# Optimization experiments

Hardware: AMD Instinct MI355X
Metric: run time of the kernel (lower is better)

The kernel has to match this reference:

```python
import jax, jax.numpy as jnp
import numpy as np

NUM_LAYERS = 25
INPUT = 500
HIDDEN = 64
SEQ = 25
BATCH = 4096
OUT = 10
GATES = 4 * HIDDEN


def setup_inputs() -> dict:
    key = jax.random.key(0)
    ks = jax.random.split(key, 11)
    s = 0.1  # ~ uniform(-1/sqrt(H),1/sqrt(H)) scale used by torch LSTM init
    return {
        "x": jax.random.normal(ks[0], (SEQ, BATCH, INPUT), jnp.float32),
        "W_ih0": jax.random.normal(ks[1], (GATES, INPUT), jnp.float32) * s,
        "W_hh0": jax.random.normal(ks[2], (GATES, HIDDEN), jnp.float32) * s,
        "b_ih0": jax.random.normal(ks[3], (GATES,), jnp.float32) * s,
        "b_hh0": jax.random.normal(ks[4], (GATES,), jnp.float32) * s,
        "W_ih_rest": jax.random.normal(ks[5], (NUM_LAYERS - 1, GATES, HIDDEN), jnp.float32) * s,
        "W_hh_rest": jax.random.normal(ks[6], (NUM_LAYERS - 1, GATES, HIDDEN), jnp.float32) * s,
        "b_ih_rest": jax.random.normal(ks[7], (NUM_LAYERS - 1, GATES), jnp.float32) * s,
        "b_hh_rest": jax.random.normal(ks[8], (NUM_LAYERS - 1, GATES), jnp.float32) * s,
        "W_lin": jax.random.normal(ks[9], (OUT, HIDDEN), jnp.float32) * s,
        "b_lin": jax.random.normal(ks[10], (OUT,), jnp.float32) * s,
    }


def _lstm_layer(seq, Wih, Whh, bih, bhh):
    # seq: [T, B, D_in] -> (outputs [T, B, H], h_T [B, H], c_T [B, H])
    T, B, _ = seq.shape
    H = Whh.shape[1]
    # precompute input projection for all timesteps in one big GEMM
    xp = jnp.einsum('tbi,gi->tbg', seq, Wih) + bih + bhh  # [T, B, 4H]
    h0 = jnp.zeros((B, H), seq.dtype)
    c0 = jnp.zeros((B, H), seq.dtype)

    def step(carry, xpt):
        h, c = carry
        g = xpt + h @ Whh.T  # [B, 4H], torch gate order i, f, g, o
        i, f, gg, o = jnp.split(g, 4, axis=-1)
        c = jax.nn.sigmoid(f) * c + jax.nn.sigmoid(i) * jnp.tanh(gg)
        h = jax.nn.sigmoid(o) * jnp.tanh(c)
        return (h, c), h

    (hT, cT), hs = jax.lax.scan(step, (h0, c0), xp)
    return hs, hT, cT


def reference(x, W_ih0, W_hh0, b_ih0, b_hh0, W_ih_rest, W_hh_rest, b_ih_rest, b_hh_rest, W_lin, b_lin):
    hs, hT, cT = _lstm_layer(x, W_ih0, W_hh0, b_ih0, b_hh0)
    h_list, c_list = [hT], [cT]
    for l in range(NUM_LAYERS - 1):  # fixed small layer count: Python loop ok
        hs, hT, cT = _lstm_layer(hs, W_ih_rest[l], W_hh_rest[l], b_ih_rest[l], b_hh_rest[l])
        h_list.append(hT)
        c_list.append(cT)
    h_n = jnp.stack(h_list)  # [L, B, H]
    c_n = jnp.stack(c_list)  # [L, B, H]
    # faithful to torch: out[:, -1, :] indexes the BATCH dim -> [T, H]
    lstm_out = hs[:, -1, :] @ W_lin.T + b_lin  # [T, OUT]
    return (lstm_out, h_n, c_n)
```

## Files before the change

### kernel.cpp

```cpp
#include <hip/hip_runtime.h>

#define T_SEQ 25
#define NBATCH 4096
#define D_IN 500
#define HID 64
#define NG 256
#define NLAYERS 25
#define NOUT 10

typedef __attribute__((ext_vector_type(8))) short bf16x8;
typedef __attribute__((ext_vector_type(4))) short bf16x4;
typedef __attribute__((ext_vector_type(4))) float f32x4;

#define LOG2E 1.4426950408889634f

__device__ __forceinline__ short f2bf(float f) {
    union { float f; unsigned u; } v; v.f = f;
    unsigned u = v.u + 0x7FFFu + ((v.u >> 16) & 1u);
    return (short)(u >> 16);
}
__device__ __forceinline__ float bf2f(short s) {
    union { unsigned u; float f; } v;
    v.u = ((unsigned)(unsigned short)s) << 16;
    return v.f;
}
__device__ __forceinline__ bf16x8 cvt8(f32x4 a, f32x4 b) {
    bf16x8 r;
    r[0]=f2bf(a[0]); r[1]=f2bf(a[1]); r[2]=f2bf(a[2]); r[3]=f2bf(a[3]);
    r[4]=f2bf(b[0]); r[5]=f2bf(b[1]); r[6]=f2bf(b[2]); r[7]=f2bf(b[3]);
    return r;
}
__device__ __forceinline__ float sigm(float x) {
    return __builtin_amdgcn_rcpf(1.f + __builtin_amdgcn_exp2f(-LOG2E * x));
}
__device__ __forceinline__ float tanh_f(float x) {
    return 1.f - 2.f * __builtin_amdgcn_rcpf(__builtin_amdgcn_exp2f(2.f * LOG2E * x) + 1.f);
}

__global__ __launch_bounds__(256)
void prep(const float* __restrict__ Wih0, const float* __restrict__ Whh0,
          const float* __restrict__ WihR, const float* __restrict__ WhhR,
          const float* __restrict__ bihR, const float* __restrict__ bhhR,
          short* __restrict__ wbf, short* __restrict__ whh0b,
          short* __restrict__ wihRb, short* __restrict__ whhRb,
          float* __restrict__ bsum) {
    int idx = blockIdx.x * 256 + threadIdx.x;
    if (idx < 131072) {
        int row = idx >> 9, k = idx & 511;
        wbf[idx] = (k < D_IN) ? f2bf(Wih0[row * D_IN + k]) : (short)0;
    } else if (idx < 147456) {
        int j = idx - 131072; whh0b[j] = f2bf(Whh0[j]);
    } else if (idx < 540672) {
        int j = idx - 147456; wihRb[j] = f2bf(WihR[j]);
    } else if (idx < 933888) {
        int j = idx - 540672; whhRb[j] = f2bf(WhhR[j]);
    } else if (idx < 940032) {
        int j = idx - 933888; bsum[j] = bihR[j] + bhhR[j];
    }
}

__global__ __launch_bounds__(256, 1)
void xp0_gemm(const float* __restrict__ x, const short* __restrict__ wbf,
              const float* __restrict__ bih0, const float* __restrict__ bhh0,
              short* __restrict__ xp0b) {
    const int tid = threadIdx.x;
    const int wv = tid >> 6, lane = tid & 63, col = lane & 15, q = lane >> 4;
    const int t  = blockIdx.x >> 5;
    const int b0 = (blockIdx.x & 31) << 7;

    f32x4 acc[2][16];
    #pragma unroll
    for (int nt = 0; nt < 16; nt++) {
        int g = nt*16 + col;
        float bv = bih0[g] + bhh0[g];
        acc[0][nt] = (f32x4){bv,bv,bv,bv};
        acc[1][nt] = acc[0][nt];
    }
    const float* xrow0 = x + ((size_t)t*NBATCH + b0 + wv*32 + col)*D_IN;
    const float* xrow1 = xrow0 + 16*(size_t)D_IN;

    #pragma unroll 3
    for (int kc = 0; kc < 15; kc++) {
        const int ko = kc*32 + q*8;
        const f32x4* p0 = (const f32x4*)(xrow0 + ko);
        const f32x4* p1 = (const f32x4*)(xrow1 + ko);
        bf16x8 a0 = cvt8(p0[0], p0[1]);
        bf16x8 a1 = cvt8(p1[0], p1[1]);
        #pragma unroll
        for (int nt = 0; nt < 16; nt++) {
            bf16x8 bfr = *(const bf16x8*)(wbf + (size_t)(nt*16+col)*512 + kc*32 + q*8);
            acc[0][nt] = __builtin_amdgcn_mfma_f32_16x16x32_bf16(a0, bfr, acc[0][nt], 0,0,0);
            acc[1][nt] = __builtin_amdgcn_mfma_f32_16x16x32_bf16(a1, bfr, acc[1][nt], 0,0,0);
        }
    }
    {
        f32x4 z = (f32x4){0.f,0.f,0.f,0.f};
        f32x4 lo0=z, hi0=z, lo1=z, hi1=z;
        const int ko = 480 + q*8;
        if (q < 2) {
            lo0 = *(const f32x4*)(xrow0 + ko); hi0 = *(const f32x4*)(xrow0 + ko + 4);
            lo1 = *(const f32x4*)(xrow1 + ko); hi1 = *(const f32x4*)(xrow1 + ko + 4);
        } else if (q == 2) {
            lo0 = *(const f32x4*)(xrow0 + 496);
            lo1 = *(const f32x4*)(xrow1 + 496);
        }
        bf16x8 a0 = cvt8(lo0, hi0);
        bf16x8 a1 = cvt8(lo1, hi1);
        #pragma unroll
        for (int nt = 0; nt < 16; nt++) {
            bf16x8 bfr = *(const bf16x8*)(wbf + (size_t)(nt*16+col)*512 + 480 + q*8);
            acc[0][nt] = __builtin_amdgcn_mfma_f32_16x16x32_bf16(a0, bfr, acc[0][nt], 0,0,0);
            acc[1][nt] = __builtin_amdgcn_mfma_f32_16x16x32_bf16(a1, bfr, acc[1][nt], 0,0,0);
        }
    }
    #pragma unroll
    for (int ms = 0; ms < 2; ms++) {
        #pragma unroll
        for (int nt = 0; nt < 16; nt++) {
            int g = nt*16 + col;
            int b = b0 + wv*32 + ms*16 + q*4;
            bf16x4 o;
            o[0]=f2bf(acc[ms][nt][0]); o[1]=f2bf(acc[ms][nt][1]);
            o[2]=f2bf(acc[ms][nt][2]); o[3]=f2bf(acc[ms][nt][3]);
            *(bf16x4*)(xp0b + ((size_t)t*NG + g)*NBATCH + b) = o;
        }
    }
}

__global__ __launch_bounds__(256, 1)
void lstm_persist(const short* __restrict__ whh0b, const short* __restrict__ wihRb,
                  const short* __restrict__ whhRb, const float* __restrict__ bsum,
                  const float* __restrict__ Wlin, const float* __restrict__ blin,
                  const short* __restrict__ xp0b, float* __restrict__ out) {
    __shared__ short seq[T_SEQ * 16 * 72];
    const int tid = threadIdx.x;
    const int wv = tid >> 6, lane = tid & 63, col = lane & 15, q = lane >> 4;
    const int b0 = blockIdx.x << 4;
    const int hh = wv*16 + col;
    float* __restrict__ h_n = out + 250;
    float* __restrict__ c_n = out + 250 + (size_t)NLAYERS*NBATCH*HID;

    bf16x8 wih[4][2], whh[4][2];
    float bias[4];

    #pragma unroll 1
    for (int l = 0; l < NLAYERS; l++) {
        if (l == 0) {
            #pragma unroll
            for (int gt = 0; gt < 4; gt++) {
                const short* wr = whh0b + (size_t)(gt*64 + hh)*64;
                whh[gt][0] = *(const bf16x8*)(wr + q*8);
                whh[gt][1] = *(const bf16x8*)(wr + 32 + q*8);
            }
        } else {
            const short* wi = wihRb + (size_t)(l-1)*16384;
            const short* wh = whhRb + (size_t)(l-1)*16384;
            #pragma unroll
            for (int gt = 0; gt < 4; gt++) {
                int g = gt*64 + hh;
                wih[gt][0] = *(const bf16x8*)(wi + (size_t)g*64 + q*8);
                wih[gt][1] = *(const bf16x8*)(wi + (size_t)g*64 + 32 + q*8);
                whh[gt][0] = *(const bf16x8*)(wh + (size_t)g*64 + q*8);
                whh[gt][1] = *(const bf16x8*)(wh + (size_t)g*64 + 32 + q*8);
                bias[gt] = bsum[(size_t)(l-1)*NG + g];
            }
        }
        float c[4] = {0.f, 0.f, 0.f, 0.f};

        #pragma unroll 1
        for (int j = 0; j < 5; j++) {
            const int t0 = j*5;
            f32x4 pre[5][4];
            if (l == 0) {
                #pragma unroll
                for (int i = 0; i < 5; i++) {
                    #pragma unroll
                    for (int gt = 0; gt < 4; gt++) {
                        bf16x4 v = *(const bf16x4*)(xp0b +
                            ((size_t)(t0+i)*NG + gt*64 + hh)*NBATCH + b0 + q*4);
                        f32x4 p;
                        p[0]=bf2f(v[0]); p[1]=bf2f(v[1]); p[2]=bf2f(v[2]); p[3]=bf2f(v[3]);
                        pre[i][gt] = p;
                    }
                }
            } else {
                #pragma unroll
                for (int i = 0; i < 5; i++) {
                    const short* sp = &seq[((t0+i)*16 + col)*72];
                    bf16x8 a0 = *(const bf16x8*)(sp + q*8);
                    bf16x8 a1 = *(const bf16x8*)(sp + 32 + q*8);
                    #pragma unroll
                    for (int gt = 0; gt < 4; gt++) {
                        f32x4 p = (f32x4){bias[gt],bias[gt],bias[gt],bias[gt]};
                        p = __builtin_amdgcn_mfma_f32_16x16x32_bf16(a0, wih[gt][0], p, 0,0,0);
                        p = __builtin_amdgcn_mfma_f32_16x16x32_bf16(a1, wih[gt][1], p, 0,0,0);
                        pre[i][gt] = p;
                    }
                }
            }
            __syncthreads();

            #pragma unroll
            for (int i = 0; i < 5; i++) {
                const int t = t0 + i;
                f32x4 acc4[4];
                #pragma unroll
                for (int gt = 0; gt < 4; gt++) acc4[gt] = pre[i][gt];
                if (i > 0 || j > 0) {
                    const short* hp = &seq[((t-1)*16 + col)*72];
                    bf16x8 h0 = *(const bf16x8*)(hp + q*8);
                    bf16x8 h1 = *(const bf16x8*)(hp + 32 + q*8);
                    #pragma unroll
                    for (int gt = 0; gt < 4; gt++) {
                        acc4[gt] = __builtin_amdgcn_mfma_f32_16x16x32_bf16(h0, whh[gt][0], acc4[gt], 0,0,0);
                        acc4[gt] = __builtin_amdgcn_mfma_f32_16x16x32_bf16(h1, whh[gt][1], acc4[gt], 0,0,0);
                    }
                }
                #pragma unroll
                for (int r = 0; r < 4; r++) {
                    float ig = sigm(acc4[0][r]);
                    float fg = sigm(acc4[1][r]);
                    float gg = tanh_f(acc4[2][r]);
                    float og = sigm(acc4[3][r]);
                    float cn = fg*c[r] + ig*gg;
                    c[r] = cn;
                    float hn = og * tanh_f(cn);
                    seq[(t*16 + q*4 + r)*72 + hh] = f2bf(hn);
                    if (i == 4) {
                        if (t == T_SEQ-1) {
                            size_t o = ((size_t)l*NBATCH + b0 + q*4 + r)*HID + hh;
                            h_n[o] = hn;
                            c_n[o] = cn;
                        }
                    }
                }
                __syncthreads();
            }
        }
    }
    if (b0 == NBATCH - 16 && tid < T_SEQ*NOUT) {
        int ti = tid / NOUT, o = tid - ti*NOUT;
        float s = blin[o];
        #pragma unroll
        for (int k = 0; k < HID; k++)
            s += bf2f(seq[(ti*16 + 15)*72 + k]) * Wlin[o*HID + k];
        out[tid] = s;
    }
}

extern "C" void kernel_launch(void* const* d_in, const int* in_sizes, int n_in,
                              void* d_out, int out_size, void* d_ws, size_t ws_size,
                              hipStream_t stream) {
    const float* x    = (const float*)d_in[0];
    const float* Wih0 = (const float*)d_in[1];
    const float* Whh0 = (const float*)d_in[2];
    const float* bih0 = (const float*)d_in[3];
    const float* bhh0 = (const float*)d_in[4];
    const float* WihR = (const float*)d_in[5];
    const float* WhhR = (const float*)d_in[6];
    const float* bihR = (const float*)d_in[7];
    const float* bhhR = (const float*)d_in[8];
    const float* Wlin = (const float*)d_in[9];
    const float* blin = (const float*)d_in[10];
    float* out = (float*)d_out;

    short* xp0b  = (short*)d_ws;
    short* wbf   = xp0b  + 26214400;
    short* whh0b = wbf   + 131072;
    short* wihRb = whh0b + 16384;
    short* whhRb = wihRb + 393216;
    float* bsum  = (float*)(whhRb + 393216);

    prep<<<dim3(3672), dim3(256), 0, stream>>>(Wih0, Whh0, WihR, WhhR, bihR, bhhR,
                                               wbf, whh0b, wihRb, whhRb, bsum);
    xp0_gemm<<<dim3(800), dim3(256), 0, stream>>>(x, wbf, bih0, bhh0, xp0b);
    lstm_persist<<<dim3(NBATCH/16), dim3(256), 0, stream>>>(
        whh0b, wihRb, whhRb, bsum, Wlin, blin, xp0b, out);
}
```

Measured before the change: 834.9 us.

## Pipeline LSTM layers in pairs across two wave groups with ring-buffered hidden states

```diff
diff --git a/kernel.cpp b/kernel.cpp
--- a/kernel.cpp
+++ b/kernel.cpp
@@ -13,6 +13,8 @@
 typedef __attribute__((ext_vector_type(4))) float f32x4;
 
 #define LOG2E 1.4426950408889634f
+#define ROWS 1152
+#define RNG_OFF 57600
 
 __device__ __forceinline__ short f2bf(float f) {
     union { float f; unsigned u; } v; v.f = f;
@@ -30,24 +32,20 @@
     r[4]=f2bf(b[0]); r[5]=f2bf(b[1]); r[6]=f2bf(b[2]); r[7]=f2bf(b[3]);
     return r;
 }
-__device__ __forceinline__ float sigm(float x) {
-    return __builtin_amdgcn_rcpf(1.f + __builtin_amdgcn_exp2f(-LOG2E * x));
-}
-__device__ __forceinline__ float tanh_f(float x) {
-    return 1.f - 2.f * __builtin_amdgcn_rcpf(__builtin_amdgcn_exp2f(2.f * LOG2E * x) + 1.f);
-}
 
 __global__ __launch_bounds__(256)
 void prep(const float* __restrict__ Wih0, const float* __restrict__ Whh0,
           const float* __restrict__ WihR, const float* __restrict__ WhhR,
           const float* __restrict__ bihR, const float* __restrict__ bhhR,
-          short* __restrict__ wbf, short* __restrict__ whh0b,
+          short* __restrict__ wbf2, short* __restrict__ whh0b,
           short* __restrict__ wihRb, short* __restrict__ whhRb,
           float* __restrict__ bsum) {
     int idx = blockIdx.x * 256 + threadIdx.x;
     if (idx < 131072) {
-        int row = idx >> 9, k = idx & 511;
-        wbf[idx] = (k < D_IN) ? f2bf(Wih0[row * D_IN + k]) : (short)0;
+        int j = idx & 7, lane = (idx >> 3) & 63, nt = (idx >> 9) & 15, kc = idx >> 13;
+        int n = nt*16 + (lane & 15);
+        int k = kc*32 + (lane >> 4)*8 + j;
+        wbf2[idx] = (k < D_IN) ? f2bf(Wih0[n * D_IN + k]) : (short)0;
     } else if (idx < 147456) {
         int j = idx - 131072; whh0b[j] = f2bf(Whh0[j]);
     } else if (idx < 540672) {
@@ -60,7 +58,7 @@
 }
 
 __global__ __launch_bounds__(256, 1)
-void xp0_gemm(const float* __restrict__ x, const short* __restrict__ wbf,
+void xp0_gemm(const float* __restrict__ x, const short* __restrict__ wbf2,
               const float* __restrict__ bih0, const float* __restrict__ bhh0,
               short* __restrict__ xp0b) {
     const int tid = threadIdx.x;
@@ -88,7 +86,7 @@
         bf16x8 a1 = cvt8(p1[0], p1[1]);
         #pragma unroll
         for (int nt = 0; nt < 16; nt++) {
-            bf16x8 bfr = *(const bf16x8*)(wbf + (size_t)(nt*16+col)*512 + kc*32 + q*8);
+            bf16x8 bfr = *(const bf16x8*)(wbf2 + ((size_t)(kc*16+nt)*64 + lane)*8);
             acc[0][nt] = __builtin_amdgcn_mfma_f32_16x16x32_bf16(a0, bfr, acc[0][nt], 0,0,0);
             acc[1][nt] = __builtin_amdgcn_mfma_f32_16x16x32_bf16(a1, bfr, acc[1][nt], 0,0,0);
         }
@@ -108,7 +106,7 @@
         bf16x8 a1 = cvt8(lo1, hi1);
         #pragma unroll
         for (int nt = 0; nt < 16; nt++) {
-            bf16x8 bfr = *(const bf16x8*)(wbf + (size_t)(nt*16+col)*512 + 480 + q*8);
+            bf16x8 bfr = *(const bf16x8*)(wbf2 + ((size_t)(15*16+nt)*64 + lane)*8);
             acc[0][nt] = __builtin_amdgcn_mfma_f32_16x16x32_bf16(a0, bfr, acc[0][nt], 0,0,0);
             acc[1][nt] = __builtin_amdgcn_mfma_f32_16x16x32_bf16(a1, bfr, acc[1][nt], 0,0,0);
         }
@@ -127,123 +125,153 @@
     }
 }
 
-__global__ __launch_bounds__(256, 1)
+
+#define GATES(ACC, OUTB, LAYER, TT)                                            \
+    do {                                                                       \
+        _Pragma("unroll")                                                      \
+        for (int rr = 0; rr < 4; rr++) {                                       \
+            float iv = ACC[0][rr], fv = ACC[1][rr];                            \
+            float gv = ACC[2][rr], ov = ACC[3][rr];                            \
+            float gc = fminf(fmaxf(gv, -30.f), 30.f);                          \
+            float ei = __builtin_amdgcn_exp2f(-LOG2E * iv);                    \
+            float eg = __builtin_amdgcn_exp2f((2.f*LOG2E) * gc);               \
+            float ef = __builtin_amdgcn_exp2f(-LOG2E * fv);                    \
+            float it = (eg - 1.f) *                                            \
+                __builtin_amdgcn_rcpf((1.f + ei) * (1.f + eg));                \
+            float cn = __builtin_amdgcn_rcpf(1.f + ef) * c4[rr] + it;          \
+            c4[rr] = cn;                                                       \
+            float cc = fminf(fmaxf(cn, -30.f), 30.f);                          \
+            float eo = __builtin_amdgcn_exp2f(-LOG2E * ov);                    \
+            float ec = __builtin_amdgcn_exp2f((2.f*LOG2E) * cc);               \
+            float hn = (ec - 1.f) *                                            \
+                __builtin_amdgcn_rcpf((1.f + eo) * (1.f + ec));                \
+            lds[(OUTB) + (q*4+rr)*72 + hh] = f2bf(hn);                         \
+            if ((TT) == 24) {                                                  \
+                size_t oi = ((size_t)(LAYER)*NBATCH + b0 + q*4 + rr)*HID + hh; \
+                h_n[oi] = hn; c_n[oi] = cn;                                    \
+            }                                                                  \
+        }                                                                      \
+    } while (0)
+
+__global__ __launch_bounds__(512, 1)
 void lstm_persist(const short* __restrict__ whh0b, const short* __restrict__ wihRb,
                   const short* __restrict__ whhRb, const float* __restrict__ bsum,
                   const float* __restrict__ Wlin, const float* __restrict__ blin,
                   const short* __restrict__ xp0b, float* __restrict__ out) {
-    __shared__ short seq[T_SEQ * 16 * 72];
+    __shared__ short lds[2*T_SEQ*ROWS + 4*ROWS];
     const int tid = threadIdx.x;
     const int wv = tid >> 6, lane = tid & 63, col = lane & 15, q = lane >> 4;
-    const int b0 = blockIdx.x << 4;
-    const int hh = wv*16 + col;
+    const int grp = wv >> 2;
+    const int hh  = (wv & 3)*16 + col;
+    const int b0  = blockIdx.x << 4;
     float* __restrict__ h_n = out + 250;
     float* __restrict__ c_n = out + 250 + (size_t)NLAYERS*NBATCH*HID;
 
+    int pOff = T_SEQ*ROWS, oOff = 0;
     bf16x8 wih[4][2], whh[4][2];
     float bias[4];
-
-    #pragma unroll 1
-    for (int l = 0; l < NLAYERS; l++) {
-        if (l == 0) {
+    float c4[4] = {0.f,0.f,0.f,0.f};
+
+    bf16x4 xpn[4];
+    if (grp == 0) {
+        #pragma unroll
+        for (int gt = 0; gt < 4; gt++) {
+            const short* wr = whh0b + (size_t)(gt*64 + hh)*64;
+            whh[gt][0] = *(const bf16x8*)(wr + q*8);
+            whh[gt][1] = *(const bf16x8*)(wr + 32 + q*8);
+            xpn[gt] = *(const bf16x4*)(xp0b + ((size_t)(gt*64 + hh))*NBATCH + b0 + q*4);
+        }
+    }
+    for (int t = 0; t < T_SEQ; t++) {
+        if (grp == 0) {
+            f32x4 acc[4];
             #pragma unroll
             for (int gt = 0; gt < 4; gt++) {
-                const short* wr = whh0b + (size_t)(gt*64 + hh)*64;
-                whh[gt][0] = *(const bf16x8*)(wr + q*8);
-                whh[gt][1] = *(const bf16x8*)(wr + 32 + q*8);
+                f32x4 p;
+                p[0]=bf2f(xpn[gt][0]); p[1]=bf2f(xpn[gt][1]);
+                p[2]=bf2f(xpn[gt][2]); p[3]=bf2f(xpn[gt][3]);
+                acc[gt] = p;
             }
-        } else {
-            const short* wi = wihRb + (size_t)(l-1)*16384;
-            const short* wh = whhRb + (size_t)(l-1)*16384;
-            #pragma unroll
-            for (int gt = 0; gt < 4; gt++) {
-                int g = gt*64 + hh;
-                wih[gt][0] = *(const bf16x8*)(wi + (size_t)g*64 + q*8);
-                wih[gt][1] = *(const bf16x8*)(wi + (size_t)g*64 + 32 + q*8);
-                whh[gt][0] = *(const bf16x8*)(wh + (size_t)g*64 + q*8);
-                whh[gt][1] = *(const bf16x8*)(wh + (size_t)g*64 + 32 + q*8);
-                bias[gt] = bsum[(size_t)(l-1)*NG + g];
+            if (t < T_SEQ-1) {
+                #pragma unroll
+                for (int gt = 0; gt < 4; gt++)
+                    xpn[gt] = *(const bf16x4*)(xp0b + (((size_t)(t+1))*NG + gt*64 + hh)*NBATCH + b0 + q*4);
             }
-        }
-        float c[4] = {0.f, 0.f, 0.f, 0.f};
+            if (t > 0) {
+                const int rb = oOff + (t-1)*ROWS + col*72;
+                bf16x8 h0 = *(const bf16x8*)&lds[rb + q*8];
+                bf16x8 h1 = *(const bf16x8*)&lds[rb + 32 + q*8];
+                #pragma unroll
+                for (int gt = 0; gt < 4; gt++) {
+                    acc[gt] = __builtin_amdgcn_mfma_f32_16x16x32_bf16(h0, whh[gt][0], acc[gt], 0,0,0);
+                    acc[gt] = __builtin_amdgcn_mfma_f32_16x16x32_bf16(h1, whh[gt][1], acc[gt], 0,0,0);
+                }
+            }
+            const int ob = oOff + t*ROWS;
+            GATES(acc, ob, 0, t);
+        }
+        __syncthreads();
+    }
+
+    #pragma unroll 1
+    for (int r = 0; r < 12; r++) {
+        { int tm = pOff; pOff = oOff; oOff = tm; }
+        const int myl = grp ? (2*r + 2) : (2*r + 1);
+        const short* wi = wihRb + (size_t)(myl-1)*16384;
+        const short* wh = whhRb + (size_t)(myl-1)*16384;
+        #pragma unroll
+        for (int gt = 0; gt < 4; gt++) {
+            int g = gt*64 + hh;
+            wih[gt][0] = *(const bf16x8*)(wi + (size_t)g*64 + q*8);
+            wih[gt][1] = *(const bf16x8*)(wi + (size_t)g*64 + 32 + q*8);
+            whh[gt][0] = *(const bf16x8*)(wh + (size_t)g*64 + q*8);
+            whh[gt][1] = *(const bf16x8*)(wh + (size_t)g*64 + 32 + q*8);
+            bias[gt] = bsum[(size_t)(myl-1)*NG + g];
+        }
+        c4[0]=c4[1]=c4[2]=c4[3]=0.f;
 
         #pragma unroll 1
-        for (int j = 0; j < 5; j++) {
-            const int t0 = j*5;
-            f32x4 pre[5][4];
-            if (l == 0) {
+        for (int s = 0; s < 26; s++) {
+            const int t = s - grp;
+            if (t >= 0 && t < T_SEQ) {
+                const int in_base  = grp ? (RNG_OFF + (t&3)*ROWS) : (pOff + t*ROWS);
+                const int out_base = grp ? (oOff + t*ROWS)        : (RNG_OFF + (t&3)*ROWS);
+                f32x4 acc[4];
                 #pragma unroll
-                for (int i = 0; i < 5; i++) {
+                for (int gt = 0; gt < 4; gt++)
+                    acc[gt] = (f32x4){bias[gt],bias[gt],bias[gt],bias[gt]};
+                {
+                    const int ib = in_base + col*72;
+                    bf16x8 a0 = *(const bf16x8*)&lds[ib + q*8];
+                    bf16x8 a1 = *(const bf16x8*)&lds[ib + 32 + q*8];
                     #pragma unroll
                     for (int gt = 0; gt < 4; gt++) {
-                        bf16x4 v = *(const bf16x4*)(xp0b +
-                            ((size_t)(t0+i)*NG + gt*64 + hh)*NBATCH + b0 + q*4);
-                        f32x4 p;
-                        p[0]=bf2f(v[0]); p[1]=bf2f(v[1]); p[2]=bf2f(v[2]); p[3]=bf2f(v[3]);
-                        pre[i][gt] = p;
+                        acc[gt] = __builtin_amdgcn_mfma_f32_16x16x32_bf16(a0, wih[gt][0], acc[gt], 0,0,0);
+                        acc[gt] = __builtin_amdgcn_mfma_f32_16x16x32_bf16(a1, wih[gt][1], acc[gt], 0,0,0);
                     }
                 }
-            } else {
-                #pragma unroll
-                for (int i = 0; i < 5; i++) {
-                    const short* sp = &seq[((t0+i)*16 + col)*72];
-                    bf16x8 a0 = *(const bf16x8*)(sp + q*8);
-                    bf16x8 a1 = *(const bf16x8*)(sp + 32 + q*8);
+                if (t > 0) {
+                    const int rb = (grp ? (oOff + (t-1)*ROWS) : (RNG_OFF + ((t-1)&3)*ROWS)) + col*72;
+                    bf16x8 h0 = *(const bf16x8*)&lds[rb + q*8];
+                    bf16x8 h1 = *(const bf16x8*)&lds[rb + 32 + q*8];
                     #pragma unroll
                     for (int gt = 0; gt < 4; gt++) {
-                        f32x4 p = (f32x4){bias[gt],bias[gt],bias[gt],bias[gt]};
-                        p = __builtin_amdgcn_mfma_f32_16x16x32_bf16(a0, wih[gt][0], p, 0,0,0);
-                        p = __builtin_amdgcn_mfma_f32_16x16x32_bf16(a1, wih[gt][1], p, 0,0,0);
-                        pre[i][gt] = p;
+                        acc[gt] = __builtin_amdgcn_mfma_f32_16x16x32_bf16(h0, whh[gt][0], acc[gt], 0,0,0);
+                        acc[gt] = __builtin_amdgcn_mfma_f32_16x16x32_bf16(h1, whh[gt][1], acc[gt], 0,0,0);
                     }
                 }
+                GATES(acc, out_base, myl, t);
             }
             __syncthreads();
-
-            #pragma unroll
-            for (int i = 0; i < 5; i++) {
-                const int t = t0 + i;
-                f32x4 acc4[4];
-                #pragma unroll
-                for (int gt = 0; gt < 4; gt++) acc4[gt] = pre[i][gt];
-                if (i > 0 || j > 0) {
-                    const short* hp = &seq[((t-1)*16 + col)*72];
-                    bf16x8 h0 = *(const bf16x8*)(hp + q*8);
-                    bf16x8 h1 = *(const bf16x8*)(hp + 32 + q*8);
-                    #pragma unroll
-                    for (int gt = 0; gt < 4; gt++) {
-                        acc4[gt] = __builtin_amdgcn_mfma_f32_16x16x32_bf16(h0, whh[gt][0], acc4[gt], 0,0,0);
-                        acc4[gt] = __builtin_amdgcn_mfma_f32_16x16x32_bf16(h1, whh[gt][1], acc4[gt], 0,0,0);
-                    }
-                }
-                #pragma unroll
-                for (int r = 0; r < 4; r++) {
-                    float ig = sigm(acc4[0][r]);
-                    float fg = sigm(acc4[1][r]);
-                    float gg = tanh_f(acc4[2][r]);
-                    float og = sigm(acc4[3][r]);
-                    float cn = fg*c[r] + ig*gg;
-                    c[r] = cn;
-                    float hn = og * tanh_f(cn);
-                    seq[(t*16 + q*4 + r)*72 + hh] = f2bf(hn);
-                    if (i == 4) {
-                        if (t == T_SEQ-1) {
-                            size_t o = ((size_t)l*NBATCH + b0 + q*4 + r)*HID + hh;
-                            h_n[o] = hn;
-                            c_n[o] = cn;
-                        }
-                    }
-                }
-                __syncthreads();
-            }
-        }
-    }
-    if (b0 == NBATCH - 16 && tid < T_SEQ*NOUT) {
+        }
+    }
+
+    if (blockIdx.x == 255 && tid < T_SEQ*NOUT) {
         int ti = tid / NOUT, o = tid - ti*NOUT;
         float s = blin[o];
         #pragma unroll
         for (int k = 0; k < HID; k++)
-            s += bf2f(seq[(ti*16 + 15)*72 + k]) * Wlin[o*HID + k];
+            s += bf2f(lds[oOff + ti*ROWS + 15*72 + k]) * Wlin[o*HID + k];
         out[tid] = s;
     }
 }
@@ -265,15 +293,15 @@
     float* out = (float*)d_out;
 
     short* xp0b  = (short*)d_ws;
-    short* wbf   = xp0b  + 26214400;
-    short* whh0b = wbf   + 131072;
+    short* wbf2  = xp0b  + 26214400;
+    short* whh0b = wbf2  + 131072;
     short* wihRb = whh0b + 16384;
     short* whhRb = wihRb + 393216;
     float* bsum  = (float*)(whhRb + 393216);
 
     prep<<<dim3(3672), dim3(256), 0, stream>>>(Wih0, Whh0, WihR, WhhR, bihR, bhhR,
-                                               wbf, whh0b, wihRb, whhRb, bsum);
-    xp0_gemm<<<dim3(800), dim3(256), 0, stream>>>(x, wbf, bih0, bhh0, xp0b);
-    lstm_persist<<<dim3(NBATCH/16), dim3(256), 0, stream>>>(
+                                               wbf2, whh0b, wihRb, whhRb, bsum);
+    xp0_gemm<<<dim3(800), dim3(256), 0, stream>>>(x, wbf2, bih0, bhh0, xp0b);
+    lstm_persist<<<dim3(NBATCH/16), dim3(512), 0, stream>>>(
         whh0b, wihRb, whhRb, bsum, Wlin, blin, xp0b, out);
 }
```

Result: faster. 716.0 us (-14.2%).
